# Kernel tuning notes

Measured on AMD Instinct MI355X. Metric: run time of the kernel, lower is better.

## Reference

```python
import jax, jax.numpy as jnp
import numpy as np

B, T, D = 4, 8192, 512
E, F, CAP = 8, 2048, 4096


def setup_inputs() -> dict:
    key = jax.random.key(0)
    ks = jax.random.split(key, 6)
    s = 0.02
    return {
        "x": jax.random.normal(ks[0], (B, T, D), dtype=jnp.float32),
        "Wr": jax.random.normal(ks[1], (D, E), dtype=jnp.float32) * s,
        "W1": jax.random.normal(ks[2], (E, D, F), dtype=jnp.float32) * s,
        "b1": jax.random.normal(ks[3], (E, F), dtype=jnp.float32) * s,
        "W2": jax.random.normal(ks[4], (E, F, D), dtype=jnp.float32) * s,
        "b2": jax.random.normal(ks[5], (E, D), dtype=jnp.float32) * s,
    }


def reference(x, Wr, W1, b1, W2, b2):
    Bb, Tt, Dd = x.shape
    N = Bb * Tt
    C = min(CAP, N)
    x_flat = x.reshape(N, Dd)
    logits = x_flat @ Wr                      # [N, E]
    probs = jax.nn.softmax(logits, axis=0)    # softmax over tokens (dim=0)
    # per-expert top-C tokens
    vals, idx = jax.lax.top_k(probs.T, C)     # [E, C]
    selected = x_flat[idx]                    # [E, C, D] gather
    h = jax.nn.gelu(jnp.einsum('ecd,edf->ecf', selected, W1) + b1[:, None, :],
                    approximate=False)
    out_e = jnp.einsum('ecf,efd->ecd', h, W2) + b2[:, None, :]  # [E, C, D]
    weighted = vals[..., None] * out_e
    output = jnp.zeros_like(x_flat).at[idx.reshape(-1)].add(weighted.reshape(-1, Dd))
    return output.reshape(Bb, Tt, Dd)
```

## Files before the change

### kernel.cpp

```cpp
#include <hip/hip_runtime.h>
#include <math.h>

#define N_TOK 32768
#define DIM 512
#define NE 8
#define NF 2048
#define CCAP 4096

typedef __attribute__((ext_vector_type(4))) float floatx4;
typedef __attribute__((ext_vector_type(8))) short shortx8;
typedef __attribute__((ext_vector_type(4))) short shortx4;

__device__ __forceinline__ short f2bf(float f) {
  union { float f; unsigned u; } v; v.f = f;
  unsigned r = v.u + 0x7FFFu + ((v.u >> 16) & 1u);
  return (short)(r >> 16);
}

__device__ __forceinline__ unsigned f2key(float f) {
  union { float f; unsigned u; } v; v.f = f;
  return (v.u & 0x80000000u) ? ~v.u : (v.u | 0x80000000u);
}

__device__ __forceinline__ void gll16(const void* g, void* l) {
  __builtin_amdgcn_global_load_lds(
      (const __attribute__((address_space(1))) void*)g,
      (__attribute__((address_space(3))) void*)l, 16, 0, 0);
}

__device__ __forceinline__ float fast_gelu(float h) {
  float u = 0.7978845608f * (h + 0.044715f * h * h * h);
  float au = fabsf(u) * 2.885390082f;
  float z = __builtin_amdgcn_exp2f(au);
  float th = 1.0f - 2.0f * __builtin_amdgcn_rcpf(1.0f + z);
  th = copysignf(th, u);
  return 0.5f * h * (1.0f + th);
}

__device__ __forceinline__ void stage8_adv(const short** ap, short* dst, int t) {
#pragma unroll
  for (int i = 0; i < 8; i++) gll16(ap[i], dst + i * 2048 + t * 8);
#pragma unroll
  for (int i = 0; i < 8; i++) ap[i] += 64;
}

__device__ __forceinline__ void stage8_g2(const short* gA, short* dst, int t, int kk) {
#pragma unroll
  for (int i = 0; i < 8; i++)
    gll16(gA + (size_t)i * 32 * NF + kk * 64, dst + i * 2048 + t * 8);
}

__device__ __forceinline__ void compute64(const short* ldsA, const short* gB,
                                          floatx4 (*acc)[4], int arow, int lx, int q,
                                          int koff, int ldb) {
#pragma unroll
  for (int g = 0; g < 2; g++) {
    const int pu = (((g << 2) | q) ^ lx) << 3;
    shortx8 bf[4];
#pragma unroll
    for (int j = 0; j < 4; j++)
      bf[j] = *(const shortx8*)(gB + (size_t)j * 16 * ldb + koff + g * 32);
    shortx8 af[8];
#pragma unroll
    for (int i = 0; i < 8; i++)
      af[i] = *(const shortx8*)&ldsA[(arow + i * 16) * 64 + pu];
#pragma unroll
    for (int i = 0; i < 8; i++)
#pragma unroll
      for (int j = 0; j < 4; j++)
        acc[i][j] = __builtin_amdgcn_mfma_f32_16x16x32_bf16(af[i], bf[j], acc[i][j], 0, 0, 0);
  }
}

__global__ __launch_bounds__(256) void k_prep(
    const float* __restrict__ x, const float* __restrict__ W1,
    const float* __restrict__ W2, const float* __restrict__ Wr,
    float* __restrict__ out, short* __restrict__ xb,
    short* __restrict__ w1t, short* __restrict__ w2t,
    float* __restrict__ logitsT) {
  __shared__ float tl[64 * 68];
  const int b = blockIdx.x, t = threadIdx.x;
  if (b < 4096) {
    const float* in;
    short* o;
    int R, C, c0, r0;
    if (b < 2048) {
      int e = b >> 8, tlid = b & 255;
      in = W1 + (size_t)e * DIM * NF;
      o = w1t + (size_t)e * NF * DIM;
      R = DIM; C = NF;
      c0 = (tlid & 31) * 64; r0 = (tlid >> 5) * 64;
    } else {
      int bb = b - 2048;
      int e = bb >> 8, tlid = bb & 255;
      in = W2 + (size_t)e * NF * DIM;
      o = w2t + (size_t)e * DIM * NF;
      R = NF; C = DIM;
      c0 = (tlid & 7) * 64; r0 = (tlid >> 3) * 64;
    }
    const int r = t >> 4, cq = (t & 15) * 4;
#pragma unroll
    for (int ii = 0; ii < 4; ii++) {
      floatx4 v = *(const floatx4*)&in[(size_t)(r0 + r + 16 * ii) * C + c0 + cq];
      *(floatx4*)&tl[(r + 16 * ii) * 68 + cq] = v;
    }
    __syncthreads();
    const int cc = t >> 2, rq = (t & 3) * 16;
    shortx8 o0, o1;
#pragma unroll
    for (int k = 0; k < 8; k++) o0[k] = f2bf(tl[(rq + k) * 68 + cc]);
#pragma unroll
    for (int k = 0; k < 8; k++) o1[k] = f2bf(tl[(rq + 8 + k) * 68 + cc]);
    size_t ob = (size_t)(c0 + cc) * R + r0 + rq;
    *(shortx8*)&o[ob] = o0;
    *(shortx8*)&o[ob + 8] = o1;
  } else if (b < 4608) {
    const int base = (b - 4096) * 8192 + t;
    floatx4 z = {0.f, 0.f, 0.f, 0.f};
#pragma unroll
    for (int i = 0; i < 32; i++) *(floatx4*)&out[(size_t)(base + i * 256) * 4] = z;
  } else if (b < 5120) {
    const int base = (b - 4608) * 8192 + t;
#pragma unroll
    for (int i = 0; i < 32; i++) {
      floatx4 v = *(const floatx4*)&x[(size_t)(base + i * 256) * 4];
      shortx4 s;
      s.x = f2bf(v.x); s.y = f2bf(v.y); s.z = f2bf(v.z); s.w = f2bf(v.w);
      *(shortx4*)&xb[(size_t)(base + i * 256) * 4] = s;
    }
  } else {
    const int lane = t & 63;
    const int wave = (b - 5120) * 4 + (t >> 6);
    float wr[64];
#pragma unroll
    for (int i = 0; i < 16; i++)
      *(floatx4*)&wr[i * 4] = *(const floatx4*)&Wr[lane * 64 + i * 4];
    for (int n = wave; n < N_TOK; n += 4096) {
      const float* xr = x + (size_t)n * DIM + lane * 8;
      floatx4 x0 = *(const floatx4*)xr;
      floatx4 x1 = *(const floatx4*)(xr + 4);
      float xs[8] = {x0.x, x0.y, x0.z, x0.w, x1.x, x1.y, x1.z, x1.w};
      double acc[8];
#pragma unroll
      for (int e2 = 0; e2 < 8; e2++) acc[e2] = 0.0;
#pragma unroll
      for (int j = 0; j < 8; j++) {
        double xv = (double)xs[j];
#pragma unroll
        for (int e2 = 0; e2 < 8; e2++) acc[e2] += xv * (double)wr[j * 8 + e2];
      }
#pragma unroll
      for (int e2 = 0; e2 < 8; e2++) {
#pragma unroll
        for (int off2 = 32; off2 > 0; off2 >>= 1)
          acc[e2] += __shfl_xor(acc[e2], off2);
      }
      double rv = acc[0];
#pragma unroll
      for (int e2 = 1; e2 < 8; e2++)
        if (lane == e2) rv = acc[e2];
      if (lane < 8) logitsT[(size_t)lane * N_TOK + n] = (float)rv;
    }
  }
}

__global__ __launch_bounds__(1024) void k_select(const float* __restrict__ logitsT,
                                                 int* __restrict__ sel_idx,
                                                 float* __restrict__ sel_val) {
  __shared__ float redf[16];
  __shared__ unsigned redu[16];
  __shared__ float s_max, s_inv;
  __shared__ unsigned s_tot;
  __shared__ unsigned s_cnt[2];
  const int e = blockIdx.x, t = threadIdx.x;
  const int wid = t >> 6, lane = t & 63;
  const float* lg = logitsT + (size_t)e * N_TOK;
  float lv[32];
  unsigned kv[32];
#pragma unroll
  for (int i = 0; i < 32; i++) lv[i] = lg[i * 1024 + t];
#pragma unroll
  for (int i = 0; i < 32; i++) kv[i] = f2key(lv[i]);
  float m = lv[0];
#pragma unroll
  for (int i = 1; i < 32; i++) m = fmaxf(m, lv[i]);
#pragma unroll
  for (int o = 32; o > 0; o >>= 1) m = fmaxf(m, __shfl_xor(m, o));
  if (lane == 0) redf[wid] = m;
  __syncthreads();
  if (t == 0) {
    float v = redf[0];
    for (int i = 1; i < 16; i++) v = fmaxf(v, redf[i]);
    s_max = v;
  }
  __syncthreads();
  m = s_max;
  float s = 0.f;
#pragma unroll
  for (int i = 0; i < 32; i++) s += expf(lv[i] - m);
#pragma unroll
  for (int o = 32; o > 0; o >>= 1) s += __shfl_xor(s, o);
  if (lane == 0) redf[wid] = s;
  __syncthreads();
  if (t == 0) {
    float v = 0.f;
    for (int i = 0; i < 16; i++) v += redf[i];
    s_inv = 1.0f / v;
  }
  unsigned T = 0;
  for (int bb = 31; bb >= 0; --bb) {
    unsigned cand = T | (1u << bb);
    unsigned c = 0;
#pragma unroll
    for (int i = 0; i < 32; i++) c += (kv[i] >= cand) ? 1u : 0u;
#pragma unroll
    for (int o = 32; o > 0; o >>= 1) c += __shfl_xor(c, o);
    if (lane == 0) redu[wid] = c;
    __syncthreads();
    if (t == 0) {
      unsigned v = 0;
      for (int i = 0; i < 16; i++) v += redu[i];
      s_tot = v;
    }
    __syncthreads();
    if (s_tot >= CCAP) T = cand;
  }
  {
    unsigned c = 0;
#pragma unroll
    for (int i = 0; i < 32; i++) c += (kv[i] > T) ? 1u : 0u;
#pragma unroll
    for (int o = 32; o > 0; o >>= 1) c += __shfl_xor(c, o);
    if (lane == 0) redu[wid] = c;
    __syncthreads();
    if (t == 0) {
      unsigned v = 0;
      for (int i = 0; i < 16; i++) v += redu[i];
      s_tot = v;
      s_cnt[0] = 0;
      s_cnt[1] = 0;
    }
    __syncthreads();
  }
  const unsigned rr = CCAP - s_tot;
  const float inv = s_inv;
  const unsigned long long lmask = (1ull << lane) - 1ull;
#pragma unroll
  for (int i = 0; i < 32; i++) {
    int n = i * 1024 + t;
    bool gt = kv[i] > T;
    bool eq = kv[i] == T;
    unsigned long long mg = __ballot(gt);
    unsigned long long mq = __ballot(eq);
    unsigned bg = 0, bq = 0;
    if (lane == 0) {
      if (mg) bg = atomicAdd(&s_cnt[0], (unsigned)__popcll(mg));
      if (mq) bq = atomicAdd(&s_cnt[1], (unsigned)__popcll(mq));
    }
    bg = __shfl(bg, 0);
    bq = __shfl(bq, 0);
    int pos = -1;
    if (gt) {
      pos = (int)(bg + (unsigned)__popcll(mg & lmask));
    } else if (eq) {
      unsigned qq = bq + (unsigned)__popcll(mq & lmask);
      if (qq < rr) pos = (int)(CCAP - rr + qq);
    }
    if (pos >= 0) {
      sel_idx[e * CCAP + pos] = n;
      sel_val[e * CCAP + pos] = expf(lv[i] - m) * inv;
    }
  }
}

__global__ __launch_bounds__(256, 2) void k_gemm1(
    const short* __restrict__ xb, const short* __restrict__ w1t,
    const float* __restrict__ b1, const int* __restrict__ sel_idx,
    short* __restrict__ H, int e0) {
  __shared__ char smem[256 * 136 * 2];
  short* ldsA0 = (short*)smem;
  short* ldsA1 = (short*)(smem + 32768);

  int bx, by, zi;
  if (gridDim.z == 8) {
    int lid = blockIdx.x + (blockIdx.y << 4) + (blockIdx.z << 8);
    zi = lid & 7;
    int rem = lid >> 3;
    bx = rem & 15;
    by = rem >> 4;
  } else {
    bx = blockIdx.x; by = blockIdx.y; zi = blockIdx.z;
  }
  const int e = e0 + zi;
  const int c0 = by * 256;
  const int f0 = bx * 128;
  const int t = threadIdx.x;
  const int lane = t & 63;
  const int w = t >> 6;
  const int wm = w & 1, wn = w >> 1;
  const int row8 = t >> 3;
  const int su = (t & 7) ^ (row8 & 7);

  const short* gAp[8];
#pragma unroll
  for (int i = 0; i < 8; i++) {
    int tok = sel_idx[e * CCAP + c0 + row8 + i * 32];
    gAp[i] = xb + (size_t)tok * DIM + su * 8;
  }
  const short* gB = w1t + ((size_t)(e * NF + f0 + wn * 64 + (lane & 15))) * DIM + (lane >> 4) * 8;

  floatx4 acc[8][4];
#pragma unroll
  for (int i = 0; i < 8; i++)
#pragma unroll
    for (int j = 0; j < 4; j++) acc[i][j] = (floatx4){0.f, 0.f, 0.f, 0.f};

  const int arow = wm * 128 + (lane & 15);
  const int lx = lane & 7, q = lane >> 4;

  stage8_adv(gAp, ldsA0, t);
  __syncthreads();
  for (int kk = 0; kk < DIM / 64; kk += 2) {
    stage8_adv(gAp, ldsA1, t);
    compute64(ldsA0, gB, acc, arow, lx, q, kk * 64, DIM);
    __syncthreads();
    if (kk + 2 < DIM / 64) stage8_adv(gAp, ldsA0, t);
    compute64(ldsA1, gB, acc, arow, lx, q, (kk + 1) * 64, DIM);
    __syncthreads();
  }

  short* ep = (short*)smem;
  const int colL = wn * 64 + (lane & 15);
  const int rowL = wm * 128 + ((lane >> 4) << 2);
#pragma unroll
  for (int j = 0; j < 4; j++) {
    float bv = b1[e * NF + f0 + colL + j * 16];
#pragma unroll
    for (int i = 0; i < 8; i++) {
#pragma unroll
      for (int r = 0; r < 4; r++) {
        float h = acc[i][j][r] + bv;
        ep[(rowL + i * 16 + r) * 136 + colL + j * 16] = f2bf(fast_gelu(h));
      }
    }
  }
  __syncthreads();
  short* Hp = H + (size_t)zi * CCAP * NF;
  const int chunk = t & 15;
#pragma unroll
  for (int it = 0; it < 16; it++) {
    int r = (t >> 4) + 16 * it;
    shortx8 v = *(const shortx8*)&ep[r * 136 + chunk * 8];
    *(shortx8*)&Hp[(size_t)(c0 + r) * NF + f0 + chunk * 8] = v;
  }
}

__global__ __launch_bounds__(256, 2) void k_gemm2(
    const short* __restrict__ H, const short* __restrict__ w2t,
    const float* __restrict__ b2, const int* __restrict__ sel_idx,
    const float* __restrict__ sel_val, float* __restrict__ out, int e0) {
  __shared__ char smem[2 * 32768 + 256 * 4 + 256 * 4];
  short* ldsA0 = (short*)smem;
  short* ldsA1 = (short*)(smem + 32768);
  int* tokL = (int*)(smem + 65536);
  float* valL = (float*)(smem + 65536 + 1024);

  int bx, by, zi;
  if (gridDim.z == 8) {
    int lid = blockIdx.x + (blockIdx.y << 2) + (blockIdx.z << 6);
    zi = lid & 7;
    int rem = lid >> 3;
    bx = rem & 3;
    by = rem >> 2;
  } else {
    bx = blockIdx.x; by = blockIdx.y; zi = blockIdx.z;
  }
  const int e = e0 + zi;
  const int c0 = by * 256;
  const int d0 = bx * 128;
  const int t = threadIdx.x;
  const int lane = t & 63;
  const int w = t >> 6;
  const int wm = w & 1, wn = w >> 1;
  tokL[t] = sel_idx[e * CCAP + c0 + t];
  valL[t] = sel_val[e * CCAP + c0 + t];
  const int row8 = t >> 3;
  const int su = (t & 7) ^ (row8 & 7);

  const short* gA = H + ((size_t)zi * CCAP + c0 + row8) * NF + su * 8;
  const short* gB = w2t + ((size_t)(e * DIM + d0 + wn * 64 + (lane & 15))) * NF + (lane >> 4) * 8;

  floatx4 acc[8][4];
#pragma unroll
  for (int i = 0; i < 8; i++)
#pragma unroll
    for (int j = 0; j < 4; j++) acc[i][j] = (floatx4){0.f, 0.f, 0.f, 0.f};

  const int arow = wm * 128 + (lane & 15);
  const int lx = lane & 7, q = lane >> 4;

  stage8_g2(gA, ldsA0, t, 0);
  __syncthreads();
  for (int kk = 0; kk < NF / 64; kk += 2) {
    stage8_g2(gA, ldsA1, t, kk + 1);
    compute64(ldsA0, gB, acc, arow, lx, q, kk * 64, NF);
    __syncthreads();
    if (kk + 2 < NF / 64) stage8_g2(gA, ldsA0, t, kk + 2);
    compute64(ldsA1, gB, acc, arow, lx, q, (kk + 1) * 64, NF);
    __syncthreads();
  }

  const int colL = wn * 64 + (lane & 15);
  const int rowL = wm * 128 + ((lane >> 4) << 2);
#pragma unroll
  for (int j = 0; j < 4; j++) {
    float bv = b2[e * DIM + d0 + colL + j * 16];
#pragma unroll
    for (int i = 0; i < 8; i++) {
#pragma unroll
      for (int r = 0; r < 4; r++) {
        int row = rowL + i * 16 + r;
        float o = acc[i][j][r] + bv;
        atomicAdd(&out[(size_t)tokL[row] * DIM + d0 + colL + j * 16], valL[row] * o);
      }
    }
  }
}

extern "C" void kernel_launch(void* const* d_in, const int* in_sizes, int n_in,
                              void* d_out, int out_size, void* d_ws, size_t ws_size,
                              hipStream_t stream) {
  const float* x = (const float*)d_in[0];
  const float* Wr = (const float*)d_in[1];
  const float* W1 = (const float*)d_in[2];
  const float* b1 = (const float*)d_in[3];
  const float* W2 = (const float*)d_in[4];
  const float* b2 = (const float*)d_in[5];
  float* out = (float*)d_out;

  char* p = (char*)d_ws;
  size_t off = 0;
  auto carve = [&](size_t bytes) {
    void* r = p + off;
    off = (off + bytes + 255) & ~(size_t)255;
    return r;
  };
  short* xb = (short*)carve((size_t)N_TOK * DIM * 2);
  short* w1t = (short*)carve((size_t)NE * NF * DIM * 2);
  short* w2t = (short*)carve((size_t)NE * DIM * NF * 2);
  float* logitsT = (float*)carve((size_t)NE * N_TOK * 4);
  int* selidx = (int*)carve((size_t)NE * CCAP * 4);
  float* selval = (float*)carve((size_t)NE * CCAP * 4);
  const size_t hbytes = (size_t)CCAP * NF * 2;
  int g = 1;
  if (off + 8 * hbytes <= ws_size) g = 8;
  else if (off + 4 * hbytes <= ws_size) g = 4;
  else if (off + 2 * hbytes <= ws_size) g = 2;
  short* Hbuf = (short*)carve((size_t)g * hbytes);

  k_prep<<<6144, 256, 0, stream>>>(x, W1, W2, Wr, out, xb, w1t, w2t, logitsT);
  k_select<<<NE, 1024, 0, stream>>>(logitsT, selidx, selval);
  for (int e0 = 0; e0 < NE; e0 += g) {
    k_gemm1<<<dim3(NF / 128, CCAP / 256, g), 256, 0, stream>>>(xb, w1t, b1, selidx, Hbuf, e0);
    k_gemm2<<<dim3(DIM / 128, CCAP / 256, g), 256, 0, stream>>>(Hbuf, w2t, b2, selidx, selval, out, e0);
  }
}
```

Baseline: 557.9 us.

## Replace scatter atomics with per-token combine; register-prefetch B in GEMMs

The second GEMM now writes bf16 per-expert outputs to a buffer instead of doing float atomicAdd scatter into the output. A new combine kernel gathers each token's expert slots, recorded by k_select through a counter and slot list, and sums the weighted contributions once per token. Both GEMMs now double-buffer B fragments in registers, use a barrier that waits only on partial vmcnt, and use a generalised XCD block mapping. The changes target atomic contention and exposed global-load latency, at the cost of an extra kernel, extra workspace traffic and bf16 rounding of the expert outputs.

```diff
diff --git a/kernel.cpp b/kernel.cpp
--- a/kernel.cpp
+++ b/kernel.cpp
@@ -15,6 +15,11 @@
   union { float f; unsigned u; } v; v.f = f;
   unsigned r = v.u + 0x7FFFu + ((v.u >> 16) & 1u);
   return (short)(r >> 16);
+}
+
+__device__ __forceinline__ float bf2f(short s) {
+  union { unsigned u; float f; } v; v.u = ((unsigned)(unsigned short)s) << 16;
+  return v.f;
 }
 
 __device__ __forceinline__ unsigned f2key(float f) {
@@ -50,16 +55,19 @@
     gll16(gA + (size_t)i * 32 * NF + kk * 64, dst + i * 2048 + t * 8);
 }
 
-__device__ __forceinline__ void compute64(const short* ldsA, const short* gB,
-                                          floatx4 (*acc)[4], int arow, int lx, int q,
-                                          int koff, int ldb) {
+__device__ __forceinline__ void loadB(const short* gB, int koff, int ldb, shortx8* bf) {
+#pragma unroll
+  for (int g = 0; g < 2; g++)
+#pragma unroll
+    for (int j = 0; j < 4; j++)
+      bf[g * 4 + j] = *(const shortx8*)(gB + (size_t)j * 16 * ldb + koff + g * 32);
+}
+
+__device__ __forceinline__ void compute64r(const short* ldsA, const shortx8* bf,
+                                           floatx4 (*acc)[4], int arow, int lx, int q) {
 #pragma unroll
   for (int g = 0; g < 2; g++) {
     const int pu = (((g << 2) | q) ^ lx) << 3;
-    shortx8 bf[4];
-#pragma unroll
-    for (int j = 0; j < 4; j++)
-      bf[j] = *(const shortx8*)(gB + (size_t)j * 16 * ldb + koff + g * 32);
     shortx8 af[8];
 #pragma unroll
     for (int i = 0; i < 8; i++)
@@ -68,8 +76,24 @@
     for (int i = 0; i < 8; i++)
 #pragma unroll
       for (int j = 0; j < 4; j++)
-        acc[i][j] = __builtin_amdgcn_mfma_f32_16x16x32_bf16(af[i], bf[j], acc[i][j], 0, 0, 0);
-  }
+        acc[i][j] = __builtin_amdgcn_mfma_f32_16x16x32_bf16(af[i], bf[g * 4 + j], acc[i][j], 0, 0, 0);
+  }
+}
+
+__device__ __forceinline__ void bar_v8() {
+  asm volatile("s_waitcnt vmcnt(8) lgkmcnt(0)" ::: "memory");
+  __builtin_amdgcn_sched_barrier(0);
+  __builtin_amdgcn_s_barrier();
+}
+
+__device__ __forceinline__ void xcd_map(int& bx, int& by, int& zi) {
+  int lid = blockIdx.x + gridDim.x * (blockIdx.y + gridDim.y * blockIdx.z);
+  int k = 8 / (int)gridDim.z;
+  int x = lid & 7, rem = lid >> 3;
+  zi = x / k;
+  int bxy = rem * k + (x % k);
+  bx = bxy % (int)gridDim.x;
+  by = bxy / (int)gridDim.x;
 }
 
 __global__ __launch_bounds__(256) void k_prep(
@@ -77,7 +101,7 @@
     const float* __restrict__ W2, const float* __restrict__ Wr,
     float* __restrict__ out, short* __restrict__ xb,
     short* __restrict__ w1t, short* __restrict__ w2t,
-    float* __restrict__ logitsT) {
+    float* __restrict__ logitsT, int* __restrict__ cnt) {
   __shared__ float tl[64 * 68];
   const int b = blockIdx.x, t = threadIdx.x;
   if (b < 4096) {
@@ -128,7 +152,7 @@
       s.x = f2bf(v.x); s.y = f2bf(v.y); s.z = f2bf(v.z); s.w = f2bf(v.w);
       *(shortx4*)&xb[(size_t)(base + i * 256) * 4] = s;
     }
-  } else {
+  } else if (b < 6144) {
     const int lane = t & 63;
     const int wave = (b - 5120) * 4 + (t >> 6);
     float wr[64];
@@ -161,12 +185,17 @@
         if (lane == e2) rv = acc[e2];
       if (lane < 8) logitsT[(size_t)lane * N_TOK + n] = (float)rv;
     }
+  } else {
+#pragma unroll
+    for (int i = 0; i < 128; i++) cnt[t + 256 * i] = 0;
   }
 }
 
 __global__ __launch_bounds__(1024) void k_select(const float* __restrict__ logitsT,
                                                  int* __restrict__ sel_idx,
-                                                 float* __restrict__ sel_val) {
+                                                 float* __restrict__ sel_val,
+                                                 int* __restrict__ cnt,
+                                                 int* __restrict__ slots) {
   __shared__ float redf[16];
   __shared__ unsigned redu[16];
   __shared__ float s_max, s_inv;
@@ -269,6 +298,8 @@
     if (pos >= 0) {
       sel_idx[e * CCAP + pos] = n;
       sel_val[e * CCAP + pos] = expf(lv[i] - m) * inv;
+      int s2 = atomicAdd(&cnt[n], 1);
+      slots[n * 8 + s2] = (e << 16) | pos;
     }
   }
 }
@@ -282,15 +313,7 @@
   short* ldsA1 = (short*)(smem + 32768);
 
   int bx, by, zi;
-  if (gridDim.z == 8) {
-    int lid = blockIdx.x + (blockIdx.y << 4) + (blockIdx.z << 8);
-    zi = lid & 7;
-    int rem = lid >> 3;
-    bx = rem & 15;
-    by = rem >> 4;
-  } else {
-    bx = blockIdx.x; by = blockIdx.y; zi = blockIdx.z;
-  }
+  xcd_map(bx, by, zi);
   const int e = e0 + zi;
   const int c0 = by * 256;
   const int f0 = bx * 128;
@@ -318,17 +341,30 @@
   const int arow = wm * 128 + (lane & 15);
   const int lx = lane & 7, q = lane >> 4;
 
+  shortx8 bfA[8], bfB[8];
   stage8_adv(gAp, ldsA0, t);
-  __syncthreads();
+  __builtin_amdgcn_sched_barrier(0);
+  loadB(gB, 0, DIM, bfA);
+  bar_v8();
+
   for (int kk = 0; kk < DIM / 64; kk += 2) {
     stage8_adv(gAp, ldsA1, t);
-    compute64(ldsA0, gB, acc, arow, lx, q, kk * 64, DIM);
-    __syncthreads();
-    if (kk + 2 < DIM / 64) stage8_adv(gAp, ldsA0, t);
-    compute64(ldsA1, gB, acc, arow, lx, q, (kk + 1) * 64, DIM);
-    __syncthreads();
-  }
-
+    __builtin_amdgcn_sched_barrier(0);
+    loadB(gB, (kk + 1) * 64, DIM, bfB);
+    compute64r(ldsA0, bfA, acc, arow, lx, q);
+    bar_v8();
+    if (kk + 2 < DIM / 64) {
+      stage8_adv(gAp, ldsA0, t);
+      __builtin_amdgcn_sched_barrier(0);
+      loadB(gB, (kk + 2) * 64, DIM, bfA);
+      compute64r(ldsA1, bfB, acc, arow, lx, q);
+      bar_v8();
+    } else {
+      compute64r(ldsA1, bfB, acc, arow, lx, q);
+    }
+  }
+
+  __syncthreads();
   short* ep = (short*)smem;
   const int colL = wn * 64 + (lane & 15);
   const int rowL = wm * 128 + ((lane >> 4) << 2);
@@ -357,24 +393,13 @@
 
 __global__ __launch_bounds__(256, 2) void k_gemm2(
     const short* __restrict__ H, const short* __restrict__ w2t,
-    const float* __restrict__ b2, const int* __restrict__ sel_idx,
-    const float* __restrict__ sel_val, float* __restrict__ out, int e0) {
-  __shared__ char smem[2 * 32768 + 256 * 4 + 256 * 4];
+    const float* __restrict__ b2, short* __restrict__ oute, int e0) {
+  __shared__ char smem[256 * 136 * 2];
   short* ldsA0 = (short*)smem;
   short* ldsA1 = (short*)(smem + 32768);
-  int* tokL = (int*)(smem + 65536);
-  float* valL = (float*)(smem + 65536 + 1024);
 
   int bx, by, zi;
-  if (gridDim.z == 8) {
-    int lid = blockIdx.x + (blockIdx.y << 2) + (blockIdx.z << 6);
-    zi = lid & 7;
-    int rem = lid >> 3;
-    bx = rem & 3;
-    by = rem >> 2;
-  } else {
-    bx = blockIdx.x; by = blockIdx.y; zi = blockIdx.z;
-  }
+  xcd_map(bx, by, zi);
   const int e = e0 + zi;
   const int c0 = by * 256;
   const int d0 = bx * 128;
@@ -382,8 +407,6 @@
   const int lane = t & 63;
   const int w = t >> 6;
   const int wm = w & 1, wn = w >> 1;
-  tokL[t] = sel_idx[e * CCAP + c0 + t];
-  valL[t] = sel_val[e * CCAP + c0 + t];
   const int row8 = t >> 3;
   const int su = (t & 7) ^ (row8 & 7);
 
@@ -399,17 +422,31 @@
   const int arow = wm * 128 + (lane & 15);
   const int lx = lane & 7, q = lane >> 4;
 
+  shortx8 bfA[8], bfB[8];
   stage8_g2(gA, ldsA0, t, 0);
-  __syncthreads();
+  __builtin_amdgcn_sched_barrier(0);
+  loadB(gB, 0, NF, bfA);
+  bar_v8();
+
   for (int kk = 0; kk < NF / 64; kk += 2) {
     stage8_g2(gA, ldsA1, t, kk + 1);
-    compute64(ldsA0, gB, acc, arow, lx, q, kk * 64, NF);
-    __syncthreads();
-    if (kk + 2 < NF / 64) stage8_g2(gA, ldsA0, t, kk + 2);
-    compute64(ldsA1, gB, acc, arow, lx, q, (kk + 1) * 64, NF);
-    __syncthreads();
-  }
-
+    __builtin_amdgcn_sched_barrier(0);
+    loadB(gB, (kk + 1) * 64, NF, bfB);
+    compute64r(ldsA0, bfA, acc, arow, lx, q);
+    bar_v8();
+    if (kk + 2 < NF / 64) {
+      stage8_g2(gA, ldsA0, t, kk + 2);
+      __builtin_amdgcn_sched_barrier(0);
+      loadB(gB, (kk + 2) * 64, NF, bfA);
+      compute64r(ldsA1, bfB, acc, arow, lx, q);
+      bar_v8();
+    } else {
+      compute64r(ldsA1, bfB, acc, arow, lx, q);
+    }
+  }
+
+  __syncthreads();
+  short* ep = (short*)smem;
   const int colL = wn * 64 + (lane & 15);
   const int rowL = wm * 128 + ((lane >> 4) << 2);
 #pragma unroll
@@ -419,12 +456,45 @@
     for (int i = 0; i < 8; i++) {
 #pragma unroll
       for (int r = 0; r < 4; r++) {
-        int row = rowL + i * 16 + r;
         float o = acc[i][j][r] + bv;
-        atomicAdd(&out[(size_t)tokL[row] * DIM + d0 + colL + j * 16], valL[row] * o);
+        ep[(rowL + i * 16 + r) * 136 + colL + j * 16] = f2bf(o);
       }
     }
   }
+  __syncthreads();
+  const int chunk = t & 15;
+#pragma unroll
+  for (int it = 0; it < 16; it++) {
+    int r = (t >> 4) + 16 * it;
+    shortx8 v = *(const shortx8*)&ep[r * 136 + chunk * 8];
+    *(shortx8*)&oute[((size_t)e * CCAP + c0 + r) * DIM + d0 + chunk * 8] = v;
+  }
+}
+
+__global__ __launch_bounds__(256) void k_combine(
+    const short* __restrict__ oute, const int* __restrict__ cnt,
+    const int* __restrict__ slots, const float* __restrict__ sel_val,
+    float* __restrict__ out) {
+  const int lane = threadIdx.x & 63;
+  const int wid = threadIdx.x >> 6;
+  const int n = blockIdx.x * 4 + wid;
+  const int c = cnt[n];
+  if (c == 0) return;
+  float acc[8];
+#pragma unroll
+  for (int k = 0; k < 8; k++) acc[k] = 0.f;
+  for (int s = 0; s < c; ++s) {
+    int sl = slots[n * 8 + s];
+    int e = sl >> 16, pos = sl & 0xFFFF;
+    float val = sel_val[e * CCAP + pos];
+    shortx8 v = *(const shortx8*)&oute[((size_t)e * CCAP + pos) * DIM + lane * 8];
+#pragma unroll
+    for (int k = 0; k < 8; k++) acc[k] += val * bf2f(v[k]);
+  }
+  floatx4 o0 = {acc[0], acc[1], acc[2], acc[3]};
+  floatx4 o1 = {acc[4], acc[5], acc[6], acc[7]};
+  *(floatx4*)&out[(size_t)n * DIM + lane * 8] = o0;
+  *(floatx4*)&out[(size_t)n * DIM + lane * 8 + 4] = o1;
 }
 
 extern "C" void kernel_launch(void* const* d_in, const int* in_sizes, int n_in,
@@ -451,6 +521,9 @@
   float* logitsT = (float*)carve((size_t)NE * N_TOK * 4);
   int* selidx = (int*)carve((size_t)NE * CCAP * 4);
   float* selval = (float*)carve((size_t)NE * CCAP * 4);
+  int* cnt = (int*)carve((size_t)N_TOK * 4);
+  int* slots = (int*)carve((size_t)N_TOK * 8 * 4);
+  short* oute = (short*)carve((size_t)NE * CCAP * DIM * 2);
   const size_t hbytes = (size_t)CCAP * NF * 2;
   int g = 1;
   if (off + 8 * hbytes <= ws_size) g = 8;
@@ -458,10 +531,11 @@
   else if (off + 2 * hbytes <= ws_size) g = 2;
   short* Hbuf = (short*)carve((size_t)g * hbytes);
 
-  k_prep<<<6144, 256, 0, stream>>>(x, W1, W2, Wr, out, xb, w1t, w2t, logitsT);
-  k_select<<<NE, 1024, 0, stream>>>(logitsT, selidx, selval);
+  k_prep<<<6145, 256, 0, stream>>>(x, W1, W2, Wr, out, xb, w1t, w2t, logitsT, cnt);
+  k_select<<<NE, 1024, 0, stream>>>(logitsT, selidx, selval, cnt, slots);
   for (int e0 = 0; e0 < NE; e0 += g) {
     k_gemm1<<<dim3(NF / 128, CCAP / 256, g), 256, 0, stream>>>(xb, w1t, b1, selidx, Hbuf, e0);
-    k_gemm2<<<dim3(DIM / 128, CCAP / 256, g), 256, 0, stream>>>(Hbuf, w2t, b2, selidx, selval, out, e0);
-  }
-}
+    k_gemm2<<<dim3(DIM / 128, CCAP / 256, g), 256, 0, stream>>>(Hbuf, w2t, b2, oute, e0);
+  }
+  k_combine<<<N_TOK / 4, 256, 0, stream>>>(oute, cnt, slots, selval, out);
+}
```

Measured after the change: 1.157 ms. +107.4%, slower.
